# Performance work log

Hardware: AMD Instinct MI355X
Metric: run time of the kernel (lower is better)

The kernel has to match this reference:

```python
import jax, jax.numpy as jnp
import numpy as np

N = 50000      # nodes
E = 800000     # directed edges
P = 200000     # edge pairs to score
IN_DIM = 32
HID = 64       # per-head hidden dim
HEADS = 4
D = HID * HEADS  # 256, concat output dim
NEG_SLOPE = 0.2  # PyG GATConv leaky_relu slope


def setup_inputs() -> dict:
    key = jax.random.key(0)
    ks = jax.random.split(key, 12)
    return {
        "x": jax.random.normal(ks[0], (N, IN_DIM), jnp.float32),
        "edge_index": jax.random.randint(ks[1], (2, E), 0, N),
        "edge_pairs": jax.random.randint(ks[2], (P, 2), 0, N),
        "W1": jax.random.normal(ks[3], (IN_DIM, D), jnp.float32) / np.float32(np.sqrt(IN_DIM)),
        "att_src1": jax.random.normal(ks[4], (HEADS, HID), jnp.float32) * 0.1,
        "att_dst1": jax.random.normal(ks[5], (HEADS, HID), jnp.float32) * 0.1,
        "b1": jnp.zeros((D,), jnp.float32),
        "W2": jax.random.normal(ks[6], (D, D), jnp.float32) / np.float32(np.sqrt(D)),
        "att_src2": jax.random.normal(ks[7], (HEADS, HID), jnp.float32) * 0.1,
        "att_dst2": jax.random.normal(ks[8], (HEADS, HID), jnp.float32) * 0.1,
        "b2": jnp.zeros((D,), jnp.float32),
        "head_w": jax.random.normal(ks[9], (2 * D, 1), jnp.float32) / np.float32(np.sqrt(2 * D)),
        "head_b": jnp.zeros((1,), jnp.float32),
    }


def _gat_layer(x, src, dst, W, a_src, a_dst, b):
    """PyG-style GATConv (concat=True, self-loops already appended to src/dst)."""
    n = x.shape[0]
    h = (x @ W).reshape(n, HEADS, HID)            # [N,H,C]
    alpha_s = (h * a_src).sum(-1)                  # [N,H]
    alpha_d = (h * a_dst).sum(-1)                  # [N,H]
    e = jax.nn.leaky_relu(alpha_s[src] + alpha_d[dst], NEG_SLOPE)  # [E',H]
    # segment softmax over edges grouped by destination node
    m = jax.ops.segment_max(e, dst, num_segments=n)                # [N,H]
    ex = jnp.exp(e - m[dst])
    denom = jax.ops.segment_sum(ex, dst, num_segments=n)           # [N,H]
    alpha = ex / (denom[dst] + 1e-16)                              # [E',H]
    msg = h[src] * alpha[..., None]                                # [E',H,C]
    out = jax.ops.segment_sum(msg, dst, num_segments=n)            # [N,H,C]
    return out.reshape(n, D) + b


def reference(x, edge_index, edge_pairs, W1, att_src1, att_dst1, b1,
              W2, att_src2, att_dst2, b2, head_w, head_b):
    n = x.shape[0]
    loops = jnp.arange(n, dtype=edge_index.dtype)  # add_self_loops (PyG default)
    src = jnp.concatenate([edge_index[0], loops])
    dst = jnp.concatenate([edge_index[1], loops])
    h = jax.nn.relu(_gat_layer(x, src, dst, W1, att_src1, att_dst1, b1))
    h = jax.nn.relu(_gat_layer(h, src, dst, W2, att_src2, att_dst2, b2))
    pair = jnp.concatenate([h[edge_pairs[:, 0]], h[edge_pairs[:, 1]]], axis=1)  # [P,2D]
    return (pair @ head_w + head_b).squeeze(-1)  # [P]
```

## Files before the change

kernel.cpp:

```cpp
#include <hip/hip_runtime.h>

#define N_NODES 50000
#define E_EDGES 800000
#define E_TOT   (E_EDGES + N_NODES)
#define P_PAIRS 200000
#define IN_DIM  32
#define HID     64
#define HEADS   4
#define D       256
#define NEG_SLOPE 0.2f
#define SCAN_BS 1024
#define LOG2E 1.4426950408889634f

typedef float    f32x4 __attribute__((ext_vector_type(4)));
typedef _Float16 h16x8 __attribute__((ext_vector_type(8)));
typedef _Float16 h16x4 __attribute__((ext_vector_type(4)));

__device__ __forceinline__ float ex2(float v) { return __builtin_amdgcn_exp2f(v); }

__device__ __forceinline__ void edge_sd(const int* __restrict__ ei, int e, int& s, int& d) {
  if (e < E_EDGES) { s = ei[e]; d = ei[E_EDGES + e]; }
  else             { s = d = e - E_EDGES; }
}

__global__ void count_k(const int* __restrict__ ei, int* __restrict__ deg) {
  int e = blockIdx.x * 256 + threadIdx.x;
  if (e >= E_TOT) return;
  int s, d; edge_sd(ei, e, s, d);
  atomicAdd(&deg[d], 1);
}

__global__ __launch_bounds__(SCAN_BS) void scan_block_k(const int* __restrict__ in,
                                                        int* __restrict__ out,
                                                        int* __restrict__ bsum, int n) {
  __shared__ int tmp[SCAN_BS];
  int g = blockIdx.x * SCAN_BS + threadIdx.x;
  tmp[threadIdx.x] = (g < n) ? in[g] : 0;
  __syncthreads();
  for (int off = 1; off < SCAN_BS; off <<= 1) {
    int t = 0;
    if ((int)threadIdx.x >= off) t = tmp[threadIdx.x - off];
    __syncthreads();
    if ((int)threadIdx.x >= off) tmp[threadIdx.x] += t;
    __syncthreads();
  }
  if (g < n) out[g] = tmp[threadIdx.x];
  if (threadIdx.x == SCAN_BS - 1) bsum[blockIdx.x] = tmp[SCAN_BS - 1];
}

__global__ void scan_top_k(int* __restrict__ bsum, int nb) {
  __shared__ int tmp[256];
  tmp[threadIdx.x] = ((int)threadIdx.x < nb) ? bsum[threadIdx.x] : 0;
  __syncthreads();
  for (int off = 1; off < 256; off <<= 1) {
    int t = 0;
    if ((int)threadIdx.x >= off) t = tmp[threadIdx.x - off];
    __syncthreads();
    if ((int)threadIdx.x >= off) tmp[threadIdx.x] += t;
    __syncthreads();
  }
  if ((int)threadIdx.x < nb) bsum[threadIdx.x] = tmp[threadIdx.x];
}

__global__ void add_off_k(const int* __restrict__ scan_out,
                          const int* __restrict__ bsum,
                          int* __restrict__ rowptr) {
  int g = blockIdx.x * 256 + threadIdx.x;
  if (g >= N_NODES) return;
  int blk = g / SCAN_BS;
  int add = blk ? bsum[blk - 1] : 0;
  rowptr[g + 1] = scan_out[g] + add;
  if (g == 0) rowptr[0] = 0;
}

__global__ void scatter_k(const int* __restrict__ ei,
                          const int* __restrict__ rowptr,
                          int* __restrict__ pos, int* __restrict__ csr) {
  int e = blockIdx.x * 256 + threadIdx.x;
  if (e >= E_TOT) return;
  int s, d; edge_sd(ei, e, s, d);
  int idx = rowptr[d] + atomicAdd(&pos[d], 1);
  csr[idx] = s;
}

__global__ void prep_wa1_k(const float* __restrict__ W1,
                           const float* __restrict__ as1,
                           const float* __restrict__ ad1,
                           float* __restrict__ wa_s, float* __restrict__ wa_d) {
  int t = threadIdx.x;
  int kk = (t >> 2) & 31, h = t & 3;
  const float* att = (t < 128) ? as1 : ad1;
  float sum = 0.f;
  for (int c = 0; c < HID; ++c) sum += W1[kk * D + h * HID + c] * att[h * HID + c];
  float* dst = (t < 128) ? wa_s : wa_d;
  dst[kk * 4 + h] = sum * LOG2E;
}

__global__ void prep_w2t_k(const float* __restrict__ W2,
                           _Float16* __restrict__ Wt) {
  int g = blockIdx.x * 256 + threadIdx.x;
  int col = g >> 8, k = g & 255;
  Wt[g] = (_Float16)W2[(size_t)k * D + col];
}

__global__ __launch_bounds__(256) void alphas1_k(const float* __restrict__ x,
                                                 const float* __restrict__ wa_s,
                                                 const float* __restrict__ wa_d,
                                                 float* __restrict__ alps,
                                                 float* __restrict__ alpd) {
  int w = (blockIdx.x * 256 + threadIdx.x) >> 6;
  int lane = threadIdx.x & 63;
  int n = w * 8 + (lane >> 3);
  int j = lane & 7;
  float4 xv = make_float4(0.f, 0.f, 0.f, 0.f);
  if (n < N_NODES) xv = *(const float4*)(x + (size_t)n * IN_DIM + j * 4);
  float ps[4] = {0.f, 0.f, 0.f, 0.f}, pd[4] = {0.f, 0.f, 0.f, 0.f};
  #pragma unroll
  for (int kk = 0; kk < 4; ++kk) {
    float xk = ((const float*)&xv)[kk];
    float4 ws = *(const float4*)(wa_s + (j * 4 + kk) * 4);
    float4 wd = *(const float4*)(wa_d + (j * 4 + kk) * 4);
    ps[0] += xk * ws.x; ps[1] += xk * ws.y; ps[2] += xk * ws.z; ps[3] += xk * ws.w;
    pd[0] += xk * wd.x; pd[1] += xk * wd.y; pd[2] += xk * wd.z; pd[3] += xk * wd.w;
  }
  #pragma unroll
  for (int off = 1; off < 8; off <<= 1) {
    #pragma unroll
    for (int h = 0; h < 4; ++h) {
      ps[h] += __shfl_xor(ps[h], off);
      pd[h] += __shfl_xor(pd[h], off);
    }
  }
  if (j == 0 && n < N_NODES) {
    *(float4*)(alps + n * 4) = make_float4(ps[0], ps[1], ps[2], ps[3]);
    *(float4*)(alpd + n * 4) = make_float4(pd[0], pd[1], pd[2], pd[3]);
  }
}

__global__ __launch_bounds__(256) void gat_gather1_k(
    const int* __restrict__ rowptr, const int* __restrict__ csr,
    const float* __restrict__ alps, const float* __restrict__ alpd,
    const float* __restrict__ x, float* __restrict__ agg) {
  int wid2 = (blockIdx.x * 256 + threadIdx.x) >> 6;
  int lane = threadIdx.x & 63;
  int half = lane >> 5, l = lane & 31;
  int n = wid2 * 2 + half;
  bool valid = n < N_NODES;
  int q = l >> 3;
  int kk = (l & 7) * 4;
  int beg = valid ? rowptr[n] : 0;
  int end = valid ? rowptr[n + 1] : 0;
  float ad = valid ? alpd[n * HEADS + q] : 0.f;

  float den = 0.f;
  float4 acc = make_float4(0.f, 0.f, 0.f, 0.f);

  for (int i = beg; i < end; i += 6) {
    int s[6]; bool ok[6]; float xl[6]; float4 xv[6];
    #pragma unroll
    for (int j = 0; j < 6; ++j) { ok[j] = (i + j) < end; s[j] = ok[j] ? csr[i + j] : 0; }
    #pragma unroll
    for (int j = 0; j < 6; ++j) xl[j] = alps[s[j] * HEADS + q];
    #pragma unroll
    for (int j = 0; j < 6; ++j) xv[j] = *(const float4*)(x + (size_t)s[j] * IN_DIM + kk);
    float e[6];
    #pragma unroll
    for (int j = 0; j < 6; ++j) {
      float t = xl[j] + ad;
      t = fmaxf(t, NEG_SLOPE * t);
      e[j] = ok[j] ? ex2(t) : 0.f;
    }
    den += ((e[0] + e[1]) + (e[2] + e[3])) + (e[4] + e[5]);
    #pragma unroll
    for (int j = 0; j < 6; ++j) {
      acc.x = fmaf(e[j], xv[j].x, acc.x);
      acc.y = fmaf(e[j], xv[j].y, acc.y);
      acc.z = fmaf(e[j], xv[j].z, acc.z);
      acc.w = fmaf(e[j], xv[j].w, acc.w);
    }
  }
  if (valid) {
    float inv = 1.f / (den + 1e-16f);
    float4 o = make_float4(acc.x * inv, acc.y * inv, acc.z * inv, acc.w * inv);
    *(float4*)(agg + (size_t)n * 128 + l * 4) = o;
  }
}

__global__ __launch_bounds__(256) void gemm_head1(const float* __restrict__ agg,
                                                  const float* __restrict__ W,
                                                  const float* __restrict__ b,
                                                  _Float16* __restrict__ A16) {
  __shared__ float As[32][68];
  __shared__ float Bs[32][64];
  const int row0 = blockIdx.x * 64;
  const int q = blockIdx.y;
  const int col0 = q * 64;
  const int t = threadIdx.x, tx = t & 15, ty = t >> 4;
  #pragma unroll
  for (int i = 0; i < 2; ++i) {
    int idx = t + i * 256;
    int r = idx >> 3, k4 = idx & 7;
    int rr = row0 + r;
    float4 a = make_float4(0.f, 0.f, 0.f, 0.f);
    if (rr < N_NODES) a = *(const float4*)(agg + (size_t)rr * 128 + q * 32 + k4 * 4);
    As[k4 * 4 + 0][r] = a.x;
    As[k4 * 4 + 1][r] = a.y;
    As[k4 * 4 + 2][r] = a.z;
    As[k4 * 4 + 3][r] = a.w;
  }
  #pragma unroll
  for (int i = 0; i < 2; ++i) {
    int idx = t + i * 256;
    int k = idx >> 4, c4 = idx & 15;
    *(float4*)&Bs[k][c4 * 4] = *(const float4*)(W + (size_t)k * D + col0 + c4 * 4);
  }
  __syncthreads();
  float acc[4][4] = {{0.f}};
  #pragma unroll
  for (int k = 0; k < 32; ++k) {
    float4 av = *(const float4*)&As[k][ty * 4];
    float4 bv = *(const float4*)&Bs[k][tx * 4];
    acc[0][0] += av.x * bv.x; acc[0][1] += av.x * bv.y;
    acc[0][2] += av.x * bv.z; acc[0][3] += av.x * bv.w;
    acc[1][0] += av.y * bv.x; acc[1][1] += av.y * bv.y;
    acc[1][2] += av.y * bv.z; acc[1][3] += av.y * bv.w;
    acc[2][0] += av.z * bv.x; acc[2][1] += av.z * bv.y;
    acc[2][2] += av.z * bv.z; acc[2][3] += av.z * bv.w;
    acc[3][0] += av.w * bv.x; acc[3][1] += av.w * bv.y;
    acc[3][2] += av.w * bv.z; acc[3][3] += av.w * bv.w;
  }
  float4 bv = *(const float4*)(b + col0 + tx * 4);
  const float bb[4] = {bv.x, bv.y, bv.z, bv.w};
  #pragma unroll
  for (int i = 0; i < 4; ++i) {
    int rr = row0 + ty * 4 + i;
    if (rr < N_NODES) {
      h16x4 o4;
      #pragma unroll
      for (int j = 0; j < 4; ++j)
        o4[j] = (_Float16)fmaxf(acc[i][j] + bb[j], 0.f);
      *(h16x4*)(A16 + (size_t)rr * D + col0 + tx * 4) = o4;
    }
  }
}

__global__ __launch_bounds__(256) void gemm2_mfma(
    const _Float16* __restrict__ A16, const _Float16* __restrict__ Wt,
    const float* __restrict__ asrc, const float* __restrict__ adst,
    _Float16* __restrict__ h2, float* __restrict__ alps, float* __restrict__ alpd) {
  __shared__ __attribute__((aligned(16))) _Float16 As[128][40];
  __shared__ __attribute__((aligned(16))) _Float16 Bs[128][40];
  const int row0 = blockIdx.x * 128;
  const int col0 = blockIdx.y * 128;
  const int t = threadIdx.x;
  const int wave = t >> 6, lane = t & 63;
  const int wr = wave >> 1, wc = wave & 1;
  const int lg = lane >> 4, li = lane & 15;

  f32x4 acc[4][4];
  #pragma unroll
  for (int m = 0; m < 4; ++m)
    #pragma unroll
    for (int n = 0; n < 4; ++n) acc[m][n] = (f32x4)0.f;

  for (int kc = 0; kc < D; kc += 32) {
    #pragma unroll
    for (int i = 0; i < 2; ++i) {
      int idx = t + i * 256;
      int r = idx >> 2, seg = idx & 3;
      int rr = row0 + r;
      uint4 va = make_uint4(0, 0, 0, 0);
      if (rr < N_NODES) va = *(const uint4*)(A16 + (size_t)rr * D + kc + seg * 8);
      *(uint4*)&As[r][seg * 8] = va;
      uint4 vb = *(const uint4*)(Wt + (size_t)(col0 + r) * D + kc + seg * 8);
      *(uint4*)&Bs[r][seg * 8] = vb;
    }
    __syncthreads();
    h16x8 af[4], bf[4];
    #pragma unroll
    for (int m = 0; m < 4; ++m)
      af[m] = *(const h16x8*)&As[wr * 64 + m * 16 + li][lg * 8];
    #pragma unroll
    for (int n = 0; n < 4; ++n)
      bf[n] = *(const h16x8*)&Bs[wc * 64 + n * 16 + li][lg * 8];
    #pragma unroll
    for (int m = 0; m < 4; ++m)
      #pragma unroll
      for (int n = 0; n < 4; ++n)
        acc[m][n] = __builtin_amdgcn_mfma_f32_16x16x32_f16(af[m], bf[n], acc[m][n], 0, 0, 0);
    __syncthreads();
  }

  #pragma unroll
  for (int m = 0; m < 4; ++m) {
    #pragma unroll
    for (int reg = 0; reg < 4; ++reg) {
      int rr = row0 + wr * 64 + m * 16 + lg * 4 + reg;
      if (rr < N_NODES) {
        #pragma unroll
        for (int n = 0; n < 4; ++n)
          h2[(size_t)rr * D + col0 + wc * 64 + n * 16 + li] = (_Float16)acc[m][n][reg];
      }
    }
  }

  const int q = blockIdx.y * 2 + wc;
  float wsv[4], wdv[4];
  #pragma unroll
  for (int n = 0; n < 4; ++n) {
    wsv[n] = asrc[q * HID + n * 16 + li];
    wdv[n] = adst[q * HID + n * 16 + li];
  }
  #pragma unroll
  for (int m = 0; m < 4; ++m) {
    #pragma unroll
    for (int reg = 0; reg < 4; ++reg) {
      float ps = acc[m][0][reg] * wsv[0] + acc[m][1][reg] * wsv[1]
               + acc[m][2][reg] * wsv[2] + acc[m][3][reg] * wsv[3];
      float pd = acc[m][0][reg] * wdv[0] + acc[m][1][reg] * wdv[1]
               + acc[m][2][reg] * wdv[2] + acc[m][3][reg] * wdv[3];
      #pragma unroll
      for (int off = 1; off < 16; off <<= 1) {
        ps += __shfl_xor(ps, off);
        pd += __shfl_xor(pd, off);
      }
      int rr = row0 + wr * 64 + m * 16 + lg * 4 + reg;
      if (li == 0 && rr < N_NODES) {
        alps[rr * HEADS + q] = ps * LOG2E;
        alpd[rr * HEADS + q] = pd * LOG2E;
      }
    }
  }
}

__global__ __launch_bounds__(256) void gat_gather2_k(
    const int* __restrict__ rowptr, const int* __restrict__ csr,
    const float* __restrict__ alps, const float* __restrict__ alpd,
    const _Float16* __restrict__ h, const float* __restrict__ b,
    const float* __restrict__ hw,
    float* __restrict__ u, float* __restrict__ v) {
  int wid2 = (blockIdx.x * 256 + threadIdx.x) >> 6;
  int lane = threadIdx.x & 63;
  int half = lane >> 5, l = lane & 31;
  int n = wid2 * 2 + half;
  bool valid = n < N_NODES;
  int q = l >> 3;
  int beg = valid ? rowptr[n] : 0;
  int end = valid ? rowptr[n + 1] : 0;
  float ad = valid ? alpd[n * HEADS + q] : 0.f;

  float den = 0.f;
  float acc[8] = {0.f, 0.f, 0.f, 0.f, 0.f, 0.f, 0.f, 0.f};

  for (int i = beg; i < end; i += 6) {
    int s[6]; bool ok[6]; float xl[6]; h16x8 hv[6];
    #pragma unroll
    for (int j = 0; j < 6; ++j) { ok[j] = (i + j) < end; s[j] = ok[j] ? csr[i + j] : 0; }
    #pragma unroll
    for (int j = 0; j < 6; ++j) xl[j] = alps[s[j] * HEADS + q];
    #pragma unroll
    for (int j = 0; j < 6; ++j) hv[j] = *(const h16x8*)(h + (size_t)s[j] * D + l * 8);
    float e[6];
    #pragma unroll
    for (int j = 0; j < 6; ++j) {
      float t = xl[j] + ad;
      t = fmaxf(t, NEG_SLOPE * t);
      e[j] = ok[j] ? ex2(t) : 0.f;
    }
    den += ((e[0] + e[1]) + (e[2] + e[3])) + (e[4] + e[5]);
    #pragma unroll
    for (int ch = 0; ch < 8; ++ch) {
      float a = acc[ch];
      a = fmaf((float)hv[0][ch], e[0], a);
      a = fmaf((float)hv[1][ch], e[1], a);
      a = fmaf((float)hv[2][ch], e[2], a);
      a = fmaf((float)hv[3][ch], e[3], a);
      a = fmaf((float)hv[4][ch], e[4], a);
      a = fmaf((float)hv[5][ch], e[5], a);
      acc[ch] = a;
    }
  }

  float inv = 1.f / (den + 1e-16f);
  float4 b0 = *(const float4*)(b + l * 8);
  float4 b1 = *(const float4*)(b + l * 8 + 4);
  float4 w00 = *(const float4*)(hw + l * 8);
  float4 w01 = *(const float4*)(hw + l * 8 + 4);
  float4 w10 = *(const float4*)(hw + D + l * 8);
  float4 w11 = *(const float4*)(hw + D + l * 8 + 4);
  const float* bb[2] = {(const float*)&b0, (const float*)&b1};
  const float* w0p[2] = {(const float*)&w00, (const float*)&w01};
  const float* w1p[2] = {(const float*)&w10, (const float*)&w11};
  float su = 0.f, sv = 0.f;
  #pragma unroll
  for (int ch = 0; ch < 8; ++ch) {
    float o = fmaxf(acc[ch] * inv + bb[ch >> 2][ch & 3], 0.f);
    su = fmaf(o, w0p[ch >> 2][ch & 3], su);
    sv = fmaf(o, w1p[ch >> 2][ch & 3], sv);
  }
  #pragma unroll
  for (int off = 16; off; off >>= 1) {
    su += __shfl_xor(su, off);
    sv += __shfl_xor(sv, off);
  }
  if (l == 0 && valid) { u[n] = su; v[n] = sv; }
}

__global__ void pair_lu_k(const int* __restrict__ pairs,
                          const float* __restrict__ u, const float* __restrict__ v,
                          const float* __restrict__ hb, float* __restrict__ out) {
  int g = blockIdx.x * 256 + threadIdx.x;
  if (g >= P_PAIRS) return;
  int a = pairs[g * 2], b = pairs[g * 2 + 1];
  out[g] = u[a] + v[b] + hb[0];
}

extern "C" void kernel_launch(void* const* d_in, const int* in_sizes, int n_in,
                              void* d_out, int out_size, void* d_ws, size_t ws_size,
                              hipStream_t stream) {
  const float* x    = (const float*)d_in[0];
  const int*   ei   = (const int*)d_in[1];
  const int*   prs  = (const int*)d_in[2];
  const float* W1   = (const float*)d_in[3];
  const float* as1  = (const float*)d_in[4];
  const float* ad1  = (const float*)d_in[5];
  const float* b1   = (const float*)d_in[6];
  const float* W2   = (const float*)d_in[7];
  const float* as2  = (const float*)d_in[8];
  const float* ad2  = (const float*)d_in[9];
  const float* b2   = (const float*)d_in[10];
  const float* hw   = (const float*)d_in[11];
  const float* hb   = (const float*)d_in[12];
  float* out = (float*)d_out;

  const int NPAD = 50048;

  char* w = (char*)d_ws;
  float* buf0 = (float*)w;             w += (size_t)N_NODES * D * 4;
  float* alps = (float*)w;             w += (size_t)N_NODES * HEADS * 4;
  float* alpd = (float*)w;             w += (size_t)N_NODES * HEADS * 4;
  int* rowptr = (int*)w;               w += (size_t)(N_NODES + 1) * 4;
  int* csr    = (int*)w;               w += (size_t)E_TOT * 4;
  float* uu   = (float*)w;             w += (size_t)N_NODES * 4;
  float* vv   = (float*)w;             w += (size_t)N_NODES * 4;
  float* wa_s = (float*)w;             w += 128 * 4;
  float* wa_d = (float*)w;             w += 128 * 4;
  _Float16* A16 = (_Float16*)w;        w += (size_t)NPAD * D * 2;
  _Float16* Wt  = (_Float16*)w;        w += (size_t)D * D * 2;

  _Float16* h2f16 = (_Float16*)buf0;

  int* deg      = (int*)buf0;
  int* pos      = deg + N_NODES;
  int* scan_out = pos + N_NODES;
  int* bsum     = scan_out + N_NODES;

  const int eBlk     = (E_TOT + 255) / 256;
  const int nScanBlk = (N_NODES + SCAN_BS - 1) / SCAN_BS;
  const int nBlk256  = (N_NODES + 255) / 256;
  const int a1Blk    = (N_NODES * 8 + 255) / 256;
  const int g1Blk    = ((N_NODES + 1) / 2 * 64 + 255) / 256;
  const int pairBlk  = (P_PAIRS + 255) / 256;
  const dim3 headGrid((N_NODES + 63) / 64, HEADS);
  const dim3 mfmaGrid(NPAD / 128, D / 128);

  hipMemsetAsync(deg, 0, (size_t)2 * N_NODES * 4, stream);
  count_k<<<eBlk, 256, 0, stream>>>(ei, deg);
  scan_block_k<<<nScanBlk, SCAN_BS, 0, stream>>>(deg, scan_out, bsum, N_NODES);
  scan_top_k<<<1, 256, 0, stream>>>(bsum, nScanBlk);
  add_off_k<<<nBlk256, 256, 0, stream>>>(scan_out, bsum, rowptr);
  scatter_k<<<eBlk, 256, 0, stream>>>(ei, rowptr, pos, csr);

  prep_wa1_k<<<1, 256, 0, stream>>>(W1, as1, ad1, wa_s, wa_d);
  prep_w2t_k<<<D * D / 256, 256, 0, stream>>>(W2, Wt);

  alphas1_k<<<a1Blk, 256, 0, stream>>>(x, wa_s, wa_d, alps, alpd);
  gat_gather1_k<<<g1Blk, 256, 0, stream>>>(rowptr, csr, alps, alpd, x, buf0);
  gemm_head1<<<headGrid, 256, 0, stream>>>(buf0, W1, b1, A16);

  gemm2_mfma<<<mfmaGrid, 256, 0, stream>>>(A16, Wt, as2, ad2, h2f16, alps, alpd);
  gat_gather2_k<<<g1Blk, 256, 0, stream>>>(rowptr, csr, alps, alpd, h2f16, b2, hw, uu, vv);

  pair_lu_k<<<pairBlk, 256, 0, stream>>>(prs, uu, vv, hb, out);
}
```

Measured before the change: 347.8 us.

## Record atomic ranks in count pass, merge prep kernels, widen gather unroll

The degree-count kernel now saves each edge's atomic slot, so the scatter kernel writes its CSR entry without a second round of atomics and the pos buffer memset shrinks. The two weight-prep kernels are merged into one launch to cut launch overhead. Both GAT gather loops process 8 neighbours per iteration instead of 6, putting more loads in flight at the cost of more registers. A rank array of E_TOT ints is carved out of buf0 and adds extra global traffic.

```diff
diff --git a/kernel.cpp b/kernel.cpp
--- a/kernel.cpp
+++ b/kernel.cpp
@@ -23,11 +23,12 @@
   else             { s = d = e - E_EDGES; }
 }
 
-__global__ void count_k(const int* __restrict__ ei, int* __restrict__ deg) {
+__global__ void count_k(const int* __restrict__ ei, int* __restrict__ deg,
+                        int* __restrict__ rank) {
   int e = blockIdx.x * 256 + threadIdx.x;
   if (e >= E_TOT) return;
   int s, d; edge_sd(ei, e, s, d);
-  atomicAdd(&deg[d], 1);
+  rank[e] = atomicAdd(&deg[d], 1);
 }
 
 __global__ __launch_bounds__(SCAN_BS) void scan_block_k(const int* __restrict__ in,
@@ -75,32 +76,31 @@
 
 __global__ void scatter_k(const int* __restrict__ ei,
                           const int* __restrict__ rowptr,
-                          int* __restrict__ pos, int* __restrict__ csr) {
+                          const int* __restrict__ rank, int* __restrict__ csr) {
   int e = blockIdx.x * 256 + threadIdx.x;
   if (e >= E_TOT) return;
   int s, d; edge_sd(ei, e, s, d);
-  int idx = rowptr[d] + atomicAdd(&pos[d], 1);
-  csr[idx] = s;
-}
-
-__global__ void prep_wa1_k(const float* __restrict__ W1,
-                           const float* __restrict__ as1,
-                           const float* __restrict__ ad1,
-                           float* __restrict__ wa_s, float* __restrict__ wa_d) {
-  int t = threadIdx.x;
-  int kk = (t >> 2) & 31, h = t & 3;
-  const float* att = (t < 128) ? as1 : ad1;
-  float sum = 0.f;
-  for (int c = 0; c < HID; ++c) sum += W1[kk * D + h * HID + c] * att[h * HID + c];
-  float* dst = (t < 128) ? wa_s : wa_d;
-  dst[kk * 4 + h] = sum * LOG2E;
-}
-
-__global__ void prep_w2t_k(const float* __restrict__ W2,
-                           _Float16* __restrict__ Wt) {
+  csr[rowptr[d] + rank[e]] = s;
+}
+
+__global__ void prep_k(const float* __restrict__ W1,
+                       const float* __restrict__ as1,
+                       const float* __restrict__ ad1,
+                       const float* __restrict__ W2,
+                       float* __restrict__ wa_s, float* __restrict__ wa_d,
+                       _Float16* __restrict__ Wt) {
   int g = blockIdx.x * 256 + threadIdx.x;
   int col = g >> 8, k = g & 255;
   Wt[g] = (_Float16)W2[(size_t)k * D + col];
+  if (blockIdx.x == 0) {
+    int t = threadIdx.x;
+    int kk = (t >> 2) & 31, h = t & 3;
+    const float* att = (t < 128) ? as1 : ad1;
+    float sum = 0.f;
+    for (int c = 0; c < HID; ++c) sum += W1[kk * D + h * HID + c] * att[h * HID + c];
+    float* dst = (t < 128) ? wa_s : wa_d;
+    dst[kk * 4 + h] = sum * LOG2E;
+  }
 }
 
 __global__ __launch_bounds__(256) void alphas1_k(const float* __restrict__ x,
@@ -155,24 +155,24 @@
   float den = 0.f;
   float4 acc = make_float4(0.f, 0.f, 0.f, 0.f);
 
-  for (int i = beg; i < end; i += 6) {
-    int s[6]; bool ok[6]; float xl[6]; float4 xv[6];
-    #pragma unroll
-    for (int j = 0; j < 6; ++j) { ok[j] = (i + j) < end; s[j] = ok[j] ? csr[i + j] : 0; }
-    #pragma unroll
-    for (int j = 0; j < 6; ++j) xl[j] = alps[s[j] * HEADS + q];
-    #pragma unroll
-    for (int j = 0; j < 6; ++j) xv[j] = *(const float4*)(x + (size_t)s[j] * IN_DIM + kk);
-    float e[6];
-    #pragma unroll
-    for (int j = 0; j < 6; ++j) {
+  for (int i = beg; i < end; i += 8) {
+    int s[8]; bool ok[8]; float xl[8]; float4 xv[8];
+    #pragma unroll
+    for (int j = 0; j < 8; ++j) { ok[j] = (i + j) < end; s[j] = ok[j] ? csr[i + j] : 0; }
+    #pragma unroll
+    for (int j = 0; j < 8; ++j) xl[j] = alps[s[j] * HEADS + q];
+    #pragma unroll
+    for (int j = 0; j < 8; ++j) xv[j] = *(const float4*)(x + (size_t)s[j] * IN_DIM + kk);
+    float e[8];
+    #pragma unroll
+    for (int j = 0; j < 8; ++j) {
       float t = xl[j] + ad;
       t = fmaxf(t, NEG_SLOPE * t);
       e[j] = ok[j] ? ex2(t) : 0.f;
     }
-    den += ((e[0] + e[1]) + (e[2] + e[3])) + (e[4] + e[5]);
-    #pragma unroll
-    for (int j = 0; j < 6; ++j) {
+    den += (((e[0] + e[1]) + (e[2] + e[3])) + ((e[4] + e[5]) + (e[6] + e[7])));
+    #pragma unroll
+    for (int j = 0; j < 8; ++j) {
       acc.x = fmaf(e[j], xv[j].x, acc.x);
       acc.y = fmaf(e[j], xv[j].y, acc.y);
       acc.z = fmaf(e[j], xv[j].z, acc.z);
@@ -352,31 +352,28 @@
   float den = 0.f;
   float acc[8] = {0.f, 0.f, 0.f, 0.f, 0.f, 0.f, 0.f, 0.f};
 
-  for (int i = beg; i < end; i += 6) {
-    int s[6]; bool ok[6]; float xl[6]; h16x8 hv[6];
-    #pragma unroll
-    for (int j = 0; j < 6; ++j) { ok[j] = (i + j) < end; s[j] = ok[j] ? csr[i + j] : 0; }
-    #pragma unroll
-    for (int j = 0; j < 6; ++j) xl[j] = alps[s[j] * HEADS + q];
-    #pragma unroll
-    for (int j = 0; j < 6; ++j) hv[j] = *(const h16x8*)(h + (size_t)s[j] * D + l * 8);
-    float e[6];
-    #pragma unroll
-    for (int j = 0; j < 6; ++j) {
+  for (int i = beg; i < end; i += 8) {
+    int s[8]; bool ok[8]; float xl[8]; h16x8 hv[8];
+    #pragma unroll
+    for (int j = 0; j < 8; ++j) { ok[j] = (i + j) < end; s[j] = ok[j] ? csr[i + j] : 0; }
+    #pragma unroll
+    for (int j = 0; j < 8; ++j) xl[j] = alps[s[j] * HEADS + q];
+    #pragma unroll
+    for (int j = 0; j < 8; ++j) hv[j] = *(const h16x8*)(h + (size_t)s[j] * D + l * 8);
+    float e[8];
+    #pragma unroll
+    for (int j = 0; j < 8; ++j) {
       float t = xl[j] + ad;
       t = fmaxf(t, NEG_SLOPE * t);
       e[j] = ok[j] ? ex2(t) : 0.f;
     }
-    den += ((e[0] + e[1]) + (e[2] + e[3])) + (e[4] + e[5]);
+    den += (((e[0] + e[1]) + (e[2] + e[3])) + ((e[4] + e[5]) + (e[6] + e[7])));
     #pragma unroll
     for (int ch = 0; ch < 8; ++ch) {
       float a = acc[ch];
-      a = fmaf((float)hv[0][ch], e[0], a);
-      a = fmaf((float)hv[1][ch], e[1], a);
-      a = fmaf((float)hv[2][ch], e[2], a);
-      a = fmaf((float)hv[3][ch], e[3], a);
-      a = fmaf((float)hv[4][ch], e[4], a);
-      a = fmaf((float)hv[5][ch], e[5], a);
+      #pragma unroll
+      for (int j = 0; j < 8; ++j)
+        a = fmaf((float)hv[j][ch], e[j], a);
       acc[ch] = a;
     }
   }
@@ -451,9 +448,9 @@
   _Float16* h2f16 = (_Float16*)buf0;
 
   int* deg      = (int*)buf0;
-  int* pos      = deg + N_NODES;
-  int* scan_out = pos + N_NODES;
+  int* scan_out = deg + N_NODES;
   int* bsum     = scan_out + N_NODES;
+  int* rank     = bsum + 64;
 
   const int eBlk     = (E_TOT + 255) / 256;
   const int nScanBlk = (N_NODES + SCAN_BS - 1) / SCAN_BS;
@@ -464,15 +461,14 @@
   const dim3 headGrid((N_NODES + 63) / 64, HEADS);
   const dim3 mfmaGrid(NPAD / 128, D / 128);
 
-  hipMemsetAsync(deg, 0, (size_t)2 * N_NODES * 4, stream);
-  count_k<<<eBlk, 256, 0, stream>>>(ei, deg);
+  hipMemsetAsync(deg, 0, (size_t)N_NODES * 4, stream);
+  count_k<<<eBlk, 256, 0, stream>>>(ei, deg, rank);
   scan_block_k<<<nScanBlk, SCAN_BS, 0, stream>>>(deg, scan_out, bsum, N_NODES);
   scan_top_k<<<1, 256, 0, stream>>>(bsum, nScanBlk);
   add_off_k<<<nBlk256, 256, 0, stream>>>(scan_out, bsum, rowptr);
-  scatter_k<<<eBlk, 256, 0, stream>>>(ei, rowptr, pos, csr);
-
-  prep_wa1_k<<<1, 256, 0, stream>>>(W1, as1, ad1, wa_s, wa_d);
-  prep_w2t_k<<<D * D / 256, 256, 0, stream>>>(W2, Wt);
+  scatter_k<<<eBlk, 256, 0, stream>>>(ei, rowptr, rank, csr);
+
+  prep_k<<<D * D / 256, 256, 0, stream>>>(W1, as1, ad1, W2, wa_s, wa_d, Wt);
 
   alphas1_k<<<a1Blk, 256, 0, stream>>>(x, wa_s, wa_d, alps, alpd);
   gat_gather1_k<<<g1Blk, 256, 0, stream>>>(rowptr, csr, alps, alpd, x, buf0);
```

Result: faster. 320.5 us (-7.9%).
